# Kernel tuning notes

Measured on AMD Instinct MI355X. Metric: run time of the kernel, lower is better.

Reference implementation:

```python
import jax, jax.numpy as jnp
import numpy as np

B, S, D, H = 8, 2048, 256, 4
DH = D // H
DFF = 4 * D


def setup_inputs() -> dict:
    key = jax.random.key(0)
    ks = jax.random.split(key, 32)
    w = lambda k, sh: (jax.random.normal(k, sh, jnp.float32) * 0.02)
    inp = {
        'global_feat': jax.random.normal(ks[0], (B, S, D), jnp.float32),
        'local_feat': jax.random.normal(ks[1], (B, S, D), jnp.float32),
        'text_feat': jax.random.normal(ks[2], (B, S, D), jnp.float32),
        'Wl1': w(ks[3], (D, D)), 'bl1': jnp.zeros((D,), jnp.float32),
        'Wl2': w(ks[4], (D, D)), 'bl2': jnp.zeros((D,), jnp.float32),
        'Wg': w(ks[5], (D, D)), 'bg': jnp.zeros((D,), jnp.float32),
        'Wgq': w(ks[6], (D, D)), 'bgq': jnp.zeros((D,), jnp.float32),
        'Wgk': w(ks[7], (D, D)), 'bgk': jnp.zeros((D,), jnp.float32),
        'Wgv': w(ks[8], (D, D)), 'bgv': jnp.zeros((D,), jnp.float32),
        'Wpq': w(ks[9], (D, D)), 'bpq': jnp.zeros((D,), jnp.float32),
        'Wpk': w(ks[10], (D, D)), 'bpk': jnp.zeros((D,), jnp.float32),
        'Wpv': w(ks[11], (D, D)), 'bpv': jnp.zeros((D,), jnp.float32),
        'Wd': w(ks[12], (D, D)), 'bd': jnp.zeros((D,), jnp.float32),
        'Wm1': w(ks[13], (D, DFF)), 'bm1': jnp.zeros((DFF,), jnp.float32),
        'Wm2': w(ks[14], (DFF, D)), 'bm2': jnp.zeros((D,), jnp.float32),
        'Wml': w(ks[15], (D, D)), 'bml': jnp.zeros((D,), jnp.float32),
    }
    return inp


def _heads(x):
    # [B,S,D] -> [B,H,S,DH]
    return x.reshape(B, S, H, DH).transpose(0, 2, 1, 3)


def _merge(x):
    # [B,H,S,DH] -> [B,S,D]
    return x.transpose(0, 2, 1, 3).reshape(B, S, D)


def reference(global_feat, local_feat, text_feat,
              Wl1, bl1, Wl2, bl2, Wg, bg,
              Wgq, bgq, Wgk, bgk, Wgv, bgv,
              Wpq, bpq, Wpk, bpk, Wpv, bpv,
              Wd, bd, Wm1, bm1, Wm2, bm2, Wml, bml):
    scale = 1.0 / jnp.sqrt(jnp.asarray(DH, jnp.float32))
    # embedding projections (dropout inactive in eval mode)
    dup_local = local_feat @ Wl1 + bl1      # local_embedding_1
    local = local_feat @ Wl2 + bl2          # local_embedding_2
    glob = global_feat @ Wg + bg            # global_embedding
    # global branch: Q from global, K/V from local
    gq = _heads(glob @ Wgq + bgq)
    gk = _heads(local @ Wgk + bgk)
    gv = _heads(local @ Wgv + bgv)
    # local branch: Q from duplicate local, K/V from text
    pq = _heads(dup_local @ Wpq + bpq)
    pk = _heads(text_feat @ Wpk + bpk)
    pv = _heads(text_feat @ Wpv + bpv)
    glb_probs = jax.nn.softmax(jnp.einsum('bhqd,bhkd->bhqk', gq, gk) * scale, axis=-1)
    plb_probs = jax.nn.softmax(jnp.einsum('bhqd,bhkd->bhqk', pq, pk) * scale, axis=-1)
    # bridging matmul: fuse probability maps
    plb_enhanced = jnp.einsum('bhqk,bhkl->bhql', glb_probs, plb_probs)
    glb_ctx = _merge(jnp.einsum('bhqk,bhkd->bhqd', glb_probs, gv))
    plb_ctx = _merge(jnp.einsum('bhqk,bhkd->bhqd', plb_enhanced, pv))
    out = (glb_ctx + plb_ctx) @ Wd + bd
    # GPT-style MLP (c_fc -> GELU -> c_proj)
    out = jax.nn.gelu(out @ Wm1 + bm1) @ Wm2 + bm2
    out = out @ Wml + bml
    return out
```

## Files before the change

### kernel.cpp

```cpp
#include <hip/hip_runtime.h>
#include <math.h>

#define Bn 8
#define Sn 2048
#define Dn 256
#define Hn 4
#define DHn 64
#define Mn (Bn*Sn)

typedef short bf16x8 __attribute__((ext_vector_type(8)));
typedef float f32x4  __attribute__((ext_vector_type(4)));
typedef float f32x16 __attribute__((ext_vector_type(16)));
typedef int   i32x4  __attribute__((ext_vector_type(4)));
typedef unsigned short u16;
typedef unsigned int   u32;
typedef unsigned long long u64;

#if defined(__has_builtin)
#if __has_builtin(__builtin_amdgcn_global_load_lds)
#define HAVE_GLL 1
#endif
#if __has_builtin(__builtin_amdgcn_permlane32_swap)
#define HAVE_PLS 1
#endif
#endif
#ifndef HAVE_GLL
#define HAVE_GLL 0
#endif
#ifndef HAVE_PLS
#define HAVE_PLS 0
#endif

__device__ __forceinline__ u16 f2b(float f){
    u32 u = __float_as_uint(f);
    u32 r = (u + 0x7fffu + ((u >> 16) & 1u)) >> 16;
    return (u16)r;
}
__device__ __forceinline__ float b2f(u16 h){ return __uint_as_float(((u32)h) << 16); }
__device__ __forceinline__ u32 cvtpk(float lo, float hi){
    u32 r;
    asm("v_cvt_pk_bf16_f32 %0, %1, %2" : "=v"(r) : "v"(lo), "v"(hi));
    return r;
}

__device__ __forceinline__ float gelu_f(float x){
    const float K1 = 2.3021143113f;
    const float K2 = 0.1029390163f;
    float x2 = x * x;
    float arg = fmaf(x2 * x, K2, x * K1);
    float e = exp2f(arg);
    float r = __builtin_amdgcn_rcpf(e + 1.0f);
    return x - x * r;
}

struct WtArgs {
    const float* src[13];
    int kdim[13], ndim[13], dstoff[13], t0[13];
};

__global__ __launch_bounds__(256) void prep_k(const float* __restrict__ lf, const float* __restrict__ gf,
                                              const float* __restrict__ tf,
                                              u16* __restrict__ o0, u16* __restrict__ o1, u16* __restrict__ o2,
                                              WtArgs a, u16* __restrict__ dst)
{
    __shared__ float tile[32][33];
    int bx = blockIdx.x;
    if (bx < 6144){
        int part = bx >> 11, blk = bx & 2047;
        const float* s = (part == 0) ? lf : (part == 1) ? gf : tf;
        u16* d = (part == 0) ? o0 : (part == 1) ? o1 : o2;
        size_t base = ((size_t)blk * 256 + threadIdx.x) * 8;
        float4 v0 = *(const float4*)(s + base);
        float4 v1 = *(const float4*)(s + base + 4);
        i32x4 o;
        o[0] = (int)cvtpk(v0.x, v0.y); o[1] = (int)cvtpk(v0.z, v0.w);
        o[2] = (int)cvtpk(v1.x, v1.y); o[3] = (int)cvtpk(v1.z, v1.w);
        *(i32x4*)(d + base) = o;
        return;
    }
    int tb = bx - 6144;
    int wi = 0;
    #pragma unroll
    for (int i = 1; i < 13; ++i) if (tb >= a.t0[i]) wi = i;
    int tt = tb - a.t0[wi];
    int N = a.ndim[wi], K = a.kdim[wi];
    int ntn = N >> 5;
    int tn = tt % ntn, tk = tt / ntn;
    int n0 = tn * 32, k0 = tk * 32;
    const float* src = a.src[wi];
    int r = threadIdx.x >> 5, c = threadIdx.x & 31;
    #pragma unroll
    for (int rr = 0; rr < 4; ++rr)
        tile[r*4+rr][c] = src[(size_t)(k0 + r*4 + rr) * N + n0 + c];
    __syncthreads();
    u16* out = dst + a.dstoff[wi];
    #pragma unroll
    for (int rr = 0; rr < 4; ++rr)
        out[(size_t)(n0 + r*4 + rr) * K + k0 + c] = f2b(tile[c][r*4+rr]);
}

struct Grp {
    const u16* A[5];
    const u16* Wt[5];
    const float* bias[5];
    void* C[5];
    float scale[5];
};

template<int ACT, int OUTF32>
__global__ __launch_bounds__(256, 4) void gemm_k(Grp g, int N, int K)
{
    const u16* __restrict__ A   = g.A[blockIdx.z];
    const u16* __restrict__ Wt  = g.Wt[blockIdx.z];
    const float* __restrict__ bias = g.bias[blockIdx.z];
    void* __restrict__ Cv = g.C[blockIdx.z];
    const float scale = g.scale[blockIdx.z];

    __shared__ u16 sm[2][6144];
    const int tid = threadIdx.x;
    const int w = tid >> 6, lane = tid & 63;
    const int l15 = lane & 15, l4 = lane >> 4;
    const int wr = w & 1, wc = w >> 1;
    const int bm = blockIdx.y << 6, bn = blockIdx.x << 7;
    const int xq = l4 ^ ((lane >> 1) & 3);

    f32x4 acc[4][2];
    #pragma unroll
    for (int nf = 0; nf < 4; ++nf)
        #pragma unroll
        for (int mf = 0; mf < 2; ++mf){
            acc[nf][mf][0]=0.f; acc[nf][mf][1]=0.f; acc[nf][mf][2]=0.f; acc[nf][mf][3]=0.f;
        }

    auto STAGE = [&](int buf, int kt){
        #pragma unroll
        for (int j = 0; j < 3; ++j){
            int ch = w*192 + j*64 + lane;
            int isB = ch >= 256;
            int cc  = isB ? ch - 256 : ch;
            int row = cc >> 2, q = cc & 3;
            int qs  = q ^ ((row >> 1) & 3);
            const u16* src = isB ? (Wt + (size_t)(bn + row) * K + kt + qs*8)
                                 : (A  + (size_t)(bm + row) * K + kt + qs*8);
#if HAVE_GLL
            u16* lb = &sm[buf][(size_t)(w*192 + j*64) * 8];
            __builtin_amdgcn_global_load_lds((const __attribute__((address_space(1))) void*)src,
                                             (__attribute__((address_space(3))) void*)lb, 16, 0, 0);
#else
            *(i32x4*)&sm[buf][(size_t)ch * 8] = *(const i32x4*)src;
#endif
        }
    };

    STAGE(0, 0);
    const int nk = K >> 5;
    for (int t = 0; t < nk; ++t){
        const int cur = t & 1;
        if (t + 1 < nk){
            STAGE(cur ^ 1, (t + 1) << 5);
#if HAVE_GLL
            asm volatile("s_waitcnt vmcnt(3)" ::: "memory");
#endif
        } else {
#if HAVE_GLL
            asm volatile("s_waitcnt vmcnt(0)" ::: "memory");
#endif
        }
        __builtin_amdgcn_s_barrier();
        asm volatile("" ::: "memory");

        const u16* As = sm[cur];
        const u16* Bs = sm[cur] + 2048;
        bf16x8 wf[4], af[2];
        #pragma unroll
        for (int nf = 0; nf < 4; ++nf)
            wf[nf] = *(const bf16x8*)(Bs + (size_t)(wc*64 + nf*16 + l15) * 32 + xq*8);
        #pragma unroll
        for (int mf = 0; mf < 2; ++mf)
            af[mf] = *(const bf16x8*)(As + (size_t)(wr*32 + mf*16 + l15) * 32 + xq*8);
        __builtin_amdgcn_s_setprio(1);
        #pragma unroll
        for (int nf = 0; nf < 4; ++nf)
            #pragma unroll
            for (int mf = 0; mf < 2; ++mf)
                acc[nf][mf] = __builtin_amdgcn_mfma_f32_16x16x32_bf16(wf[nf], af[mf], acc[nf][mf], 0, 0, 0);
        __builtin_amdgcn_s_setprio(0);

        asm volatile("" ::: "memory");
        __builtin_amdgcn_s_barrier();
    }

    #pragma unroll
    for (int nf = 0; nf < 4; ++nf){
        const int n0 = bn + wc*64 + nf*16 + l4*4;
        float4 b4 = *(const float4*)(bias + n0);
        #pragma unroll
        for (int mf = 0; mf < 2; ++mf){
            const int m = bm + wr*32 + mf*16 + l15;
            float r0 = (acc[nf][mf][0] + b4.x) * scale;
            float r1 = (acc[nf][mf][1] + b4.y) * scale;
            float r2 = (acc[nf][mf][2] + b4.z) * scale;
            float r3 = (acc[nf][mf][3] + b4.w) * scale;
            if (ACT){ r0 = gelu_f(r0); r1 = gelu_f(r1); r2 = gelu_f(r2); r3 = gelu_f(r3); }
            if (OUTF32){
                float4 o; o.x = r0; o.y = r1; o.z = r2; o.w = r3;
                *(float4*)((float*)Cv + (size_t)m * N + n0) = o;
            } else {
                u64 p = (u64)cvtpk(r0, r1) | ((u64)cvtpk(r2, r3) << 32);
                *(u64*)((u16*)Cv + (size_t)m * N + n0) = p;
            }
        }
    }
}

#define PSEL(idx, mm) ((((idx) >> 2) == 0) ? p0[4*((idx)&3)+(mm)] : p1[4*((idx)&3)+(mm)])

template<int FUSE>
__global__ __launch_bounds__(256, 2) void attn_k(const u16* __restrict__ Q, const u16* __restrict__ Kp,
                                                 const u16* __restrict__ Vp, u16* __restrict__ O,
                                                 const u16* __restrict__ ADD)
{
    __shared__ u16 Kl[64*72];
    __shared__ u16 Vt[64*72];
    const int tid = threadIdx.x;
    const int w = tid >> 6, lane = tid & 63;
    const int c31 = lane & 31, h = lane >> 5;
    const int bh = blockIdx.y;
    const size_t hb = (size_t)(bh >> 2) * Sn * Dn + (size_t)(bh & 3) * DHn;
    const int qb = blockIdx.x * 128;
    const int qrow = qb + w*32 + c31;

    bf16x8 qf[4];
    #pragma unroll
    for (int kc = 0; kc < 4; ++kc)
        qf[kc] = *(const bf16x8*)(Q + hb + (size_t)qrow * Dn + kc*16 + h*8);

    f32x16 ot0, ot1;
    #pragma unroll
    for (int r = 0; r < 16; ++r){ ot0[r] = 0.f; ot1[r] = 0.f; }
    float ll = 0.f;

    const int krow = tid >> 2, kq = tid & 3;
    const int vk0 = (tid & 15) * 4, vd0 = (tid >> 4) * 4;

    i32x4 kr0, kr1;
    u64 v0, v1, v2, v3;
    auto LOADKV = [&](int kt2){
        const u16* kb = Kp + hb + (size_t)(kt2 + krow) * Dn + kq*8;
        kr0 = *(const i32x4*)kb;
        kr1 = *(const i32x4*)(kb + 32);
        const u16* vb = Vp + hb + (size_t)(kt2 + vk0) * Dn + vd0;
        v0 = *(const u64*)(vb);
        v1 = *(const u64*)(vb + Dn);
        v2 = *(const u64*)(vb + 2*Dn);
        v3 = *(const u64*)(vb + 3*Dn);
    };
    LOADKV(0);

    const u32 SEL_LO = 0x05040100u, SEL_HI = 0x07060302u;

    for (int kt = 0; kt < Sn; kt += 64){
        if (kt) __syncthreads();
        *(i32x4*)&Kl[(size_t)krow*72 + kq*8]      = kr0;
        *(i32x4*)&Kl[(size_t)krow*72 + kq*8 + 32] = kr1;
        {
            u32 a0 = (u32)v0, a1 = (u32)v1, a2 = (u32)v2, a3 = (u32)v3;
            u32 b0 = (u32)(v0 >> 32), b1 = (u32)(v1 >> 32), b2 = (u32)(v2 >> 32), b3 = (u32)(v3 >> 32);
            u64 wd0 = (u64)__builtin_amdgcn_perm(a1, a0, SEL_LO) | ((u64)__builtin_amdgcn_perm(a3, a2, SEL_LO) << 32);
            u64 wd1 = (u64)__builtin_amdgcn_perm(a1, a0, SEL_HI) | ((u64)__builtin_amdgcn_perm(a3, a2, SEL_HI) << 32);
            u64 wd2 = (u64)__builtin_amdgcn_perm(b1, b0, SEL_LO) | ((u64)__builtin_amdgcn_perm(b3, b2, SEL_LO) << 32);
            u64 wd3 = (u64)__builtin_amdgcn_perm(b1, b0, SEL_HI) | ((u64)__builtin_amdgcn_perm(b3, b2, SEL_HI) << 32);
            *(u64*)&Vt[(size_t)(vd0 + 0)*72 + vk0] = wd0;
            *(u64*)&Vt[(size_t)(vd0 + 1)*72 + vk0] = wd1;
            *(u64*)&Vt[(size_t)(vd0 + 2)*72 + vk0] = wd2;
            *(u64*)&Vt[(size_t)(vd0 + 3)*72 + vk0] = wd3;
        }
        __syncthreads();
        if (kt + 64 < Sn) LOADKV(kt + 64);

        f32x16 s0, s1;
        #pragma unroll
        for (int r = 0; r < 16; ++r){ s0[r] = 0.f; s1[r] = 0.f; }
        __builtin_amdgcn_s_setprio(1);
        #pragma unroll
        for (int kc = 0; kc < 4; ++kc){
            bf16x8 k0 = *(const bf16x8*)&Kl[(size_t)c31*72 + kc*16 + h*8];
            bf16x8 k1 = *(const bf16x8*)&Kl[(size_t)(32 + c31)*72 + kc*16 + h*8];
            s0 = __builtin_amdgcn_mfma_f32_32x32x16_bf16(k0, qf[kc], s0, 0, 0, 0);
            s1 = __builtin_amdgcn_mfma_f32_32x32x16_bf16(k1, qf[kc], s1, 0, 0, 0);
        }
        __builtin_amdgcn_s_setprio(0);

        float p0[16], p1[16];
        float rs = 0.f;
        #pragma unroll
        for (int r = 0; r < 16; ++r){
            p0[r] = exp2f(s0[r]);
            p1[r] = exp2f(s1[r]);
            rs += p0[r] + p1[r];
        }
        ll += rs;

        __builtin_amdgcn_s_setprio(1);
        #pragma unroll
        for (int kc = 0; kc < 4; ++kc){
            const int iA = 2*kc, iB = 2*kc + 1;
            u32 wA0 = cvtpk(PSEL(iA,0), PSEL(iA,1));
            u32 wA1 = cvtpk(PSEL(iA,2), PSEL(iA,3));
            u32 wB0 = cvtpk(PSEL(iB,0), PSEL(iB,1));
            u32 wB1 = cvtpk(PSEL(iB,2), PSEL(iB,3));
            i32x4 pw;
#if HAVE_PLS
            {
                auto r02 = __builtin_amdgcn_permlane32_swap((int)wA0, (int)wB0, false, false);
                auto r13 = __builtin_amdgcn_permlane32_swap((int)wA1, (int)wB1, false, false);
                pw[0] = r02[0]; pw[1] = r13[0]; pw[2] = r02[1]; pw[3] = r13[1];
            }
#else
            {
                u32 s0v = h ? wA0 : wB0, s1v = h ? wA1 : wB1;
                u32 g0 = (u32)__shfl_xor((int)s0v, 32);
                u32 g1 = (u32)__shfl_xor((int)s1v, 32);
                pw[0] = (int)(h ? g0 : wA0);
                pw[1] = (int)(h ? g1 : wA1);
                pw[2] = (int)(h ? wB0 : g0);
                pw[3] = (int)(h ? wB1 : g1);
            }
#endif
            bf16x8 pb = *(bf16x8*)&pw;
            bf16x8 va  = *(const bf16x8*)&Vt[(size_t)c31*72 + kc*16 + h*8];
            bf16x8 vb2 = *(const bf16x8*)&Vt[(size_t)(32 + c31)*72 + kc*16 + h*8];
            ot0 = __builtin_amdgcn_mfma_f32_32x32x16_bf16(va,  pb, ot0, 0, 0, 0);
            ot1 = __builtin_amdgcn_mfma_f32_32x32x16_bf16(vb2, pb, ot1, 0, 0, 0);
        }
        __builtin_amdgcn_s_setprio(0);
    }

    ll += __shfl_xor(ll, 32);
    float inv = 1.0f / ll;
    #pragma unroll
    for (int rg = 0; rg < 4; ++rg){
        int d0 = 8*rg + 4*h;
        float r0 = ot0[4*rg+0]*inv, r1 = ot0[4*rg+1]*inv, r2 = ot0[4*rg+2]*inv, r3 = ot0[4*rg+3]*inv;
        float x0 = ot1[4*rg+0]*inv, x1 = ot1[4*rg+1]*inv, x2 = ot1[4*rg+2]*inv, x3 = ot1[4*rg+3]*inv;
        if (FUSE){
            u64 ga = *(const u64*)&ADD[hb + (size_t)qrow * Dn + d0];
            u64 gb = *(const u64*)&ADD[hb + (size_t)qrow * Dn + 32 + d0];
            r0 += b2f((u16)ga);         r1 += b2f((u16)(ga >> 16));
            r2 += b2f((u16)(ga >> 32)); r3 += b2f((u16)(ga >> 48));
            x0 += b2f((u16)gb);         x1 += b2f((u16)(gb >> 16));
            x2 += b2f((u16)(gb >> 32)); x3 += b2f((u16)(gb >> 48));
        }
        *(u64*)&O[hb + (size_t)qrow * Dn + d0]      = (u64)cvtpk(r0, r1) | ((u64)cvtpk(r2, r3) << 32);
        *(u64*)&O[hb + (size_t)qrow * Dn + 32 + d0] = (u64)cvtpk(x0, x1) | ((u64)cvtpk(x2, x3) << 32);
    }
}

extern "C" void kernel_launch(void* const* d_in, const int* in_sizes, int n_in,
                              void* d_out, int out_size, void* d_ws, size_t ws_size,
                              hipStream_t stream)
{
    (void)in_sizes; (void)n_in; (void)out_size; (void)ws_size;

    const float* gf  = (const float*)d_in[0];
    const float* lf  = (const float*)d_in[1];
    const float* tf  = (const float*)d_in[2];
    const float* bl1 = (const float*)d_in[4];
    const float* bl2 = (const float*)d_in[6];
    const float* bg  = (const float*)d_in[8];
    const float* bgq = (const float*)d_in[10];
    const float* bgk = (const float*)d_in[12];
    const float* bgv = (const float*)d_in[14];
    const float* bpq = (const float*)d_in[16];
    const float* bpk = (const float*)d_in[18];
    const float* bpv = (const float*)d_in[20];
    const float* bd  = (const float*)d_in[22];
    const float* bm1 = (const float*)d_in[24];
    const float* bm2 = (const float*)d_in[26];
    const float* bml = (const float*)d_in[28];

    const float C1 = 0.18033688011112042f;

    u16* ws = (u16*)d_ws;
    const size_t U = (size_t)Mn * Dn;
    u16* S[9];
    for (int i = 0; i < 9; ++i) S[i] = ws + (size_t)i * U;
    u16* wtb = ws + 9 * U;

    const int sq = 65536;
    u16* Wl1t = wtb + 0*sq;  u16* Wl2t = wtb + 1*sq;  u16* Wgt  = wtb + 2*sq;
    u16* Wgqt = wtb + 3*sq;  u16* Wgkt = wtb + 4*sq;  u16* Wgvt = wtb + 5*sq;
    u16* Wpqt = wtb + 6*sq;  u16* Wpkt = wtb + 7*sq;  u16* Wpvt = wtb + 8*sq;
    u16* Wdt  = wtb + 9*sq;  u16* Wmlt = wtb + 10*sq;
    u16* Wm1t = wtb + 720896;
    u16* Wm2t = wtb + 720896 + 262144;

    WtArgs wa;
    const int srcidx[13] = {3,5,7,9,11,13,15,17,19,21,27,23,25};
    for (int i = 0; i < 13; ++i){
        wa.src[i] = (const float*)d_in[srcidx[i]];
        wa.kdim[i] = 256; wa.ndim[i] = 256;
        wa.dstoff[i] = i * sq;
    }
    wa.kdim[11] = 256;  wa.ndim[11] = 1024; wa.dstoff[11] = 720896;
    wa.kdim[12] = 1024; wa.ndim[12] = 256;  wa.dstoff[12] = 983040;
    int acc_t = 0;
    for (int i = 0; i < 13; ++i){
        wa.t0[i] = acc_t;
        acc_t += (wa.ndim[i] >> 5) * (wa.kdim[i] >> 5);
    }
    prep_k<<<dim3(6144 + acc_t), 256, 0, stream>>>(lf, gf, tf, S[0], S[1], S[2], wa, wtb);

    auto GN = [&](const Grp& g, int ng, int N, int K, int act, int of32){
        dim3 gr(N / 128, Mn / 64, ng);
        if (act)        gemm_k<1,0><<<gr, 256, 0, stream>>>(g, N, K);
        else if (of32)  gemm_k<0,1><<<gr, 256, 0, stream>>>(g, N, K);
        else            gemm_k<0,0><<<gr, 256, 0, stream>>>(g, N, K);
    };
    auto G1 = [&](const u16* A, const u16* Wt_, const float* b, void* C, int N, int K,
                  float sc, int act, int of32){
        Grp g{};
        g.A[0] = A; g.Wt[0] = Wt_; g.bias[0] = b; g.C[0] = C; g.scale[0] = sc;
        GN(g, 1, N, K, act, of32);
    };

    {
        Grp g{};
        g.A[0] = S[0]; g.Wt[0] = Wl1t; g.bias[0] = bl1; g.C[0] = S[3]; g.scale[0] = 1.f;
        g.A[1] = S[0]; g.Wt[1] = Wl2t; g.bias[1] = bl2; g.C[1] = S[4]; g.scale[1] = 1.f;
        g.A[2] = S[1]; g.Wt[2] = Wgt;  g.bias[2] = bg;  g.C[2] = S[5]; g.scale[2] = 1.f;
        g.A[3] = S[2]; g.Wt[3] = Wpkt; g.bias[3] = bpk; g.C[3] = S[7]; g.scale[3] = 1.f;
        g.A[4] = S[2]; g.Wt[4] = Wpvt; g.bias[4] = bpv; g.C[4] = S[8]; g.scale[4] = 1.f;
        GN(g, 5, 256, 256, 0, 0);
    }
    {
        Grp g{};
        g.A[0] = S[3]; g.Wt[0] = Wpqt; g.bias[0] = bpq; g.C[0] = S[6]; g.scale[0] = C1;
        g.A[1] = S[5]; g.Wt[1] = Wgqt; g.bias[1] = bgq; g.C[1] = S[0]; g.scale[1] = C1;
        g.A[2] = S[4]; g.Wt[2] = Wgkt; g.bias[2] = bgk; g.C[2] = S[1]; g.scale[2] = 1.f;
        g.A[3] = S[4]; g.Wt[3] = Wgvt; g.bias[3] = bgv; g.C[3] = S[2]; g.scale[3] = 1.f;
        GN(g, 4, 256, 256, 0, 0);
    }

    attn_k<1><<<dim3(16, 32), 256, 0, stream>>>(S[6], S[7], S[8], S[3], S[2]);
    attn_k<0><<<dim3(16, 32), 256, 0, stream>>>(S[0], S[1], S[3], S[4], nullptr);

    G1(S[4], Wdt,  bd,  S[5], 256,  256,  1.f, 0, 0);
    G1(S[5], Wm1t, bm1, S[0], 1024, 256,  1.f, 1, 0);
    G1(S[0], Wm2t, bm2, S[6], 256,  1024, 1.f, 0, 0);
    G1(S[6], Wmlt, bml, d_out, 256, 256,  1.f, 0, 1);
}
```

Baseline: 243.0 us.

## Double-buffer attention K/V via direct-to-LDS loads and remap blocks across XCDs

The attention kernel now double-buffers K and V in shared memory. K goes straight from global memory into a swizzled LDS layout through global_load_lds, and V is transposed into the other buffer after the MFMAs, so only one barrier per tile is needed and the next tile's loads overlap the current compute. Both attention and GEMM kernels remap the linear block id so that blocks sharing the same head or rows land on the same XCD, which targets L2 reuse. The exp/row-sum loop is also recast to paired float2 adds. The cost is doubled LDS per block, which could lower occupancy, and the GEMM remap assumes power-of-two grid dimensions.

```diff
diff --git a/kernel.cpp b/kernel.cpp
--- a/kernel.cpp
+++ b/kernel.cpp
@@ -9,6 +9,7 @@
 #define Mn (Bn*Sn)
 
 typedef short bf16x8 __attribute__((ext_vector_type(8)));
+typedef float f32x2  __attribute__((ext_vector_type(2)));
 typedef float f32x4  __attribute__((ext_vector_type(4)));
 typedef float f32x16 __attribute__((ext_vector_type(16)));
 typedef int   i32x4  __attribute__((ext_vector_type(4)));
@@ -110,18 +111,28 @@
 template<int ACT, int OUTF32>
 __global__ __launch_bounds__(256, 4) void gemm_k(Grp g, int N, int K)
 {
-    const u16* __restrict__ A   = g.A[blockIdx.z];
-    const u16* __restrict__ Wt  = g.Wt[blockIdx.z];
-    const float* __restrict__ bias = g.bias[blockIdx.z];
-    void* __restrict__ Cv = g.C[blockIdx.z];
-    const float scale = g.scale[blockIdx.z];
+    const u32 gx = gridDim.x;
+    const u32 lgx = (u32)__builtin_ctz(gx);
+    const u32 total = gx * gridDim.y * gridDim.z;
+    const u32 lid = (blockIdx.z * gridDim.y + blockIdx.y) * gx + blockIdx.x;
+    const u32 nl = (lid & 7) * (total >> 3) + (lid >> 3);
+    const u32 bz = nl >> (lgx + 8);
+    const u32 r2 = nl & ((1u << (lgx + 8)) - 1u);
+    const u32 by = r2 >> lgx;
+    const u32 bx = r2 & ((1u << lgx) - 1u);
+
+    const u16* __restrict__ A   = g.A[bz];
+    const u16* __restrict__ Wt  = g.Wt[bz];
+    const float* __restrict__ bias = g.bias[bz];
+    void* __restrict__ Cv = g.C[bz];
+    const float scale = g.scale[bz];
 
     __shared__ u16 sm[2][6144];
     const int tid = threadIdx.x;
     const int w = tid >> 6, lane = tid & 63;
     const int l15 = lane & 15, l4 = lane >> 4;
     const int wr = w & 1, wc = w >> 1;
-    const int bm = blockIdx.y << 6, bn = blockIdx.x << 7;
+    const int bm = by << 6, bn = bx << 7;
     const int xq = l4 ^ ((lane >> 1) & 3);
 
     f32x4 acc[4][2];
@@ -213,21 +224,26 @@
     }
 }
 
-#define PSEL(idx, mm) ((((idx) >> 2) == 0) ? p0[4*((idx)&3)+(mm)] : p1[4*((idx)&3)+(mm)])
+#define PSEL(idx, mm) ((((idx) >> 2) == 0) ? pp0[(4*((idx)&3)+(mm))>>1][(4*((idx)&3)+(mm))&1] \
+                                           : pp1[(4*((idx)&3)+(mm))>>1][(4*((idx)&3)+(mm))&1])
 
 template<int FUSE>
 __global__ __launch_bounds__(256, 2) void attn_k(const u16* __restrict__ Q, const u16* __restrict__ Kp,
                                                  const u16* __restrict__ Vp, u16* __restrict__ O,
                                                  const u16* __restrict__ ADD)
 {
-    __shared__ u16 Kl[64*72];
-    __shared__ u16 Vt[64*72];
+    __shared__ u16 Kl[2][4096];
+    __shared__ u16 Vt[2][4608];
+
     const int tid = threadIdx.x;
     const int w = tid >> 6, lane = tid & 63;
     const int c31 = lane & 31, h = lane >> 5;
-    const int bh = blockIdx.y;
+
+    const int lid = blockIdx.x;
+    const int nl = (lid & 7) * 64 + (lid >> 3);
+    const int bh = nl >> 4;
+    const int qb = (nl & 15) << 7;
     const size_t hb = (size_t)(bh >> 2) * Sn * Dn + (size_t)(bh & 3) * DHn;
-    const int qb = blockIdx.x * 128;
     const int qrow = qb + w*32 + c31;
 
     bf16x8 qf[4];
@@ -240,43 +256,70 @@
     for (int r = 0; r < 16; ++r){ ot0[r] = 0.f; ot1[r] = 0.f; }
     float ll = 0.f;
 
-    const int krow = tid >> 2, kq = tid & 3;
+    const int kx = c31 & 7;
+    int koff0[4], koff1[4], voff0[4], voff1[4];
+    #pragma unroll
+    for (int kc = 0; kc < 4; ++kc){
+        int q = 2*kc + h;
+        koff0[kc] = c31*64        + (q ^ kx)*8;
+        koff1[kc] = (32 + c31)*64 + (q ^ kx)*8;
+        voff0[kc] = c31*72        + kc*16 + h*8;
+        voff1[kc] = (32 + c31)*72 + kc*16 + h*8;
+    }
+
     const int vk0 = (tid & 15) * 4, vd0 = (tid >> 4) * 4;
-
-    i32x4 kr0, kr1;
+    const u32 SEL_LO = 0x05040100u, SEL_HI = 0x07060302u;
+
     u64 v0, v1, v2, v3;
-    auto LOADKV = [&](int kt2){
-        const u16* kb = Kp + hb + (size_t)(kt2 + krow) * Dn + kq*8;
-        kr0 = *(const i32x4*)kb;
-        kr1 = *(const i32x4*)(kb + 32);
+    auto LOADV = [&](int kt2){
         const u16* vb = Vp + hb + (size_t)(kt2 + vk0) * Dn + vd0;
         v0 = *(const u64*)(vb);
         v1 = *(const u64*)(vb + Dn);
         v2 = *(const u64*)(vb + 2*Dn);
         v3 = *(const u64*)(vb + 3*Dn);
     };
-    LOADKV(0);
-
-    const u32 SEL_LO = 0x05040100u, SEL_HI = 0x07060302u;
-
-    for (int kt = 0; kt < Sn; kt += 64){
-        if (kt) __syncthreads();
-        *(i32x4*)&Kl[(size_t)krow*72 + kq*8]      = kr0;
-        *(i32x4*)&Kl[(size_t)krow*72 + kq*8 + 32] = kr1;
-        {
-            u32 a0 = (u32)v0, a1 = (u32)v1, a2 = (u32)v2, a3 = (u32)v3;
-            u32 b0 = (u32)(v0 >> 32), b1 = (u32)(v1 >> 32), b2 = (u32)(v2 >> 32), b3 = (u32)(v3 >> 32);
-            u64 wd0 = (u64)__builtin_amdgcn_perm(a1, a0, SEL_LO) | ((u64)__builtin_amdgcn_perm(a3, a2, SEL_LO) << 32);
-            u64 wd1 = (u64)__builtin_amdgcn_perm(a1, a0, SEL_HI) | ((u64)__builtin_amdgcn_perm(a3, a2, SEL_HI) << 32);
-            u64 wd2 = (u64)__builtin_amdgcn_perm(b1, b0, SEL_LO) | ((u64)__builtin_amdgcn_perm(b3, b2, SEL_LO) << 32);
-            u64 wd3 = (u64)__builtin_amdgcn_perm(b1, b0, SEL_HI) | ((u64)__builtin_amdgcn_perm(b3, b2, SEL_HI) << 32);
-            *(u64*)&Vt[(size_t)(vd0 + 0)*72 + vk0] = wd0;
-            *(u64*)&Vt[(size_t)(vd0 + 1)*72 + vk0] = wd1;
-            *(u64*)&Vt[(size_t)(vd0 + 2)*72 + vk0] = wd2;
-            *(u64*)&Vt[(size_t)(vd0 + 3)*72 + vk0] = wd3;
-        }
-        __syncthreads();
-        if (kt + 64 < Sn) LOADKV(kt + 64);
+    auto GLLK = [&](int buf, int kt2){
+        #pragma unroll
+        for (int j = 0; j < 2; ++j){
+            int ch = w*128 + j*64 + lane;
+            int r = ch >> 3, q = ch & 7;
+            int qs = q ^ (r & 7);
+            const u16* src = Kp + hb + (size_t)(kt2 + r) * Dn + qs*8;
+#if HAVE_GLL
+            u16* lb = &Kl[buf][(size_t)(w*128 + j*64) * 8];
+            __builtin_amdgcn_global_load_lds((const __attribute__((address_space(1))) void*)src,
+                                             (__attribute__((address_space(3))) void*)lb, 16, 0, 0);
+#else
+            *(i32x4*)&Kl[buf][(size_t)ch * 8] = *(const i32x4*)src;
+#endif
+        }
+    };
+    auto WRITEV = [&](int buf){
+        u32 a0 = (u32)v0, a1 = (u32)v1, a2 = (u32)v2, a3 = (u32)v3;
+        u32 b0 = (u32)(v0 >> 32), b1 = (u32)(v1 >> 32), b2 = (u32)(v2 >> 32), b3 = (u32)(v3 >> 32);
+        u64 wd0 = (u64)__builtin_amdgcn_perm(a1, a0, SEL_LO) | ((u64)__builtin_amdgcn_perm(a3, a2, SEL_LO) << 32);
+        u64 wd1 = (u64)__builtin_amdgcn_perm(a1, a0, SEL_HI) | ((u64)__builtin_amdgcn_perm(a3, a2, SEL_HI) << 32);
+        u64 wd2 = (u64)__builtin_amdgcn_perm(b1, b0, SEL_LO) | ((u64)__builtin_amdgcn_perm(b3, b2, SEL_LO) << 32);
+        u64 wd3 = (u64)__builtin_amdgcn_perm(b1, b0, SEL_HI) | ((u64)__builtin_amdgcn_perm(b3, b2, SEL_HI) << 32);
+        *(u64*)&Vt[buf][(size_t)(vd0 + 0)*72 + vk0] = wd0;
+        *(u64*)&Vt[buf][(size_t)(vd0 + 1)*72 + vk0] = wd1;
+        *(u64*)&Vt[buf][(size_t)(vd0 + 2)*72 + vk0] = wd2;
+        *(u64*)&Vt[buf][(size_t)(vd0 + 3)*72 + vk0] = wd3;
+    };
+
+    LOADV(0);
+    GLLK(0, 0);
+    WRITEV(0);
+    __syncthreads();
+
+    #pragma unroll 2
+    for (int t = 0; t < 32; ++t){
+        const int c = t & 1;
+        const bool more = (t < 31);
+        if (more){
+            LOADV((t + 1) << 6);
+            GLLK(c ^ 1, (t + 1) << 6);
+        }
 
         f32x16 s0, s1;
         #pragma unroll
@@ -284,22 +327,23 @@
         __builtin_amdgcn_s_setprio(1);
         #pragma unroll
         for (int kc = 0; kc < 4; ++kc){
-            bf16x8 k0 = *(const bf16x8*)&Kl[(size_t)c31*72 + kc*16 + h*8];
-            bf16x8 k1 = *(const bf16x8*)&Kl[(size_t)(32 + c31)*72 + kc*16 + h*8];
+            bf16x8 k0 = *(const bf16x8*)&Kl[c][koff0[kc]];
+            bf16x8 k1 = *(const bf16x8*)&Kl[c][koff1[kc]];
             s0 = __builtin_amdgcn_mfma_f32_32x32x16_bf16(k0, qf[kc], s0, 0, 0, 0);
             s1 = __builtin_amdgcn_mfma_f32_32x32x16_bf16(k1, qf[kc], s1, 0, 0, 0);
         }
         __builtin_amdgcn_s_setprio(0);
 
-        float p0[16], p1[16];
-        float rs = 0.f;
-        #pragma unroll
-        for (int r = 0; r < 16; ++r){
-            p0[r] = exp2f(s0[r]);
-            p1[r] = exp2f(s1[r]);
-            rs += p0[r] + p1[r];
-        }
-        ll += rs;
+        f32x2 pp0[8], pp1[8];
+        f32x2 rv = {0.f, 0.f};
+        #pragma unroll
+        for (int r = 0; r < 8; ++r){
+            pp0[r][0] = exp2f(s0[2*r]); pp0[r][1] = exp2f(s0[2*r+1]);
+            pp1[r][0] = exp2f(s1[2*r]); pp1[r][1] = exp2f(s1[2*r+1]);
+            rv += pp0[r];
+            rv += pp1[r];
+        }
+        ll += rv[0] + rv[1];
 
         __builtin_amdgcn_s_setprio(1);
         #pragma unroll
@@ -328,12 +372,15 @@
             }
 #endif
             bf16x8 pb = *(bf16x8*)&pw;
-            bf16x8 va  = *(const bf16x8*)&Vt[(size_t)c31*72 + kc*16 + h*8];
-            bf16x8 vb2 = *(const bf16x8*)&Vt[(size_t)(32 + c31)*72 + kc*16 + h*8];
+            bf16x8 va  = *(const bf16x8*)&Vt[c][voff0[kc]];
+            bf16x8 vb2 = *(const bf16x8*)&Vt[c][voff1[kc]];
             ot0 = __builtin_amdgcn_mfma_f32_32x32x16_bf16(va,  pb, ot0, 0, 0, 0);
             ot1 = __builtin_amdgcn_mfma_f32_32x32x16_bf16(vb2, pb, ot1, 0, 0, 0);
         }
         __builtin_amdgcn_s_setprio(0);
+
+        if (more) WRITEV(c ^ 1);
+        __syncthreads();
     }
 
     ll += __shfl_xor(ll, 32);
@@ -442,8 +489,8 @@
         GN(g, 4, 256, 256, 0, 0);
     }
 
-    attn_k<1><<<dim3(16, 32), 256, 0, stream>>>(S[6], S[7], S[8], S[3], S[2]);
-    attn_k<0><<<dim3(16, 32), 256, 0, stream>>>(S[0], S[1], S[3], S[4], nullptr);
+    attn_k<1><<<dim3(512), 256, 0, stream>>>(S[6], S[7], S[8], S[3], S[2]);
+    attn_k<0><<<dim3(512), 256, 0, stream>>>(S[0], S[1], S[3], S[4], nullptr);
 
     G1(S[4], Wdt,  bd,  S[5], 256,  256,  1.f, 0, 0);
     G1(S[5], Wm1t, bm1, S[0], 1024, 256,  1.f, 1, 0);
```

Result: no change. 247.1 us (+1.7%).
